# Optimization experiments

Hardware: AMD Instinct MI355X
Metric: run time of the kernel (lower is better)

Reference implementation:

```python
import jax, jax.numpy as jnp
import numpy as np

L = 10   # lattice side (hardcoded self.length)
K = 3    # kernel_size -> half_k = 1 wrap padding
FN = 4   # filter_num
B = 262144


def setup_inputs() -> dict:
    key = jax.random.key(0)
    k1, k2, k3, k4, k5 = jax.random.split(key, 5)
    v = jax.random.normal(k1, (B, L * L), dtype=jnp.float32)
    # torch default init scale ~ 1/sqrt(fan_in)
    conv_w = jax.random.normal(k2, (FN, 1, K, K), dtype=jnp.float32) / 3.0
    conv_b = jax.random.normal(k3, (FN,), dtype=jnp.float32) * 0.1
    deconv_w = jax.random.normal(k4, (FN, 1, 2, 2), dtype=jnp.float32) / 4.0
    deconv_b = jax.random.normal(k5, (1,), dtype=jnp.float32) * 0.1
    data = jnp.zeros((1,), dtype=jnp.int32)  # unused positional arg of log_psi
    return {"v": v, "conv_w": conv_w, "conv_b": conv_b,
            "deconv_w": deconv_w, "deconv_b": deconv_b, "data": data}


def _log_psi(v, conv_w, conv_b, deconv_w, deconv_b):
    b = v.shape[0]
    x = v.reshape(b, 1, L, L)
    # handmade_padding == periodic (wrap) pad of width half_k=1 on both spatial axes
    x = jnp.pad(x, ((0, 0), (0, 0), (1, 1), (1, 1)), mode="wrap")  # [B,1,12,12]
    # Conv2d(1, FN, 3), VALID -> [B,FN,10,10]
    y = jax.lax.conv_general_dilated(
        x, conv_w, window_strides=(1, 1), padding="VALID",
        dimension_numbers=("NCHW", "OIHW", "NCHW"))
    y = y + conv_b[None, :, None, None]
    # MaxPool2d(2,2): non-overlapping 2x2 -> [B,FN,5,5]
    y = y.reshape(b, FN, L // 2, 2, L // 2, 2).max(axis=(3, 5))
    # ConvTranspose2d(FN,1,kernel=2,stride=2): each input pixel -> disjoint 2x2 block
    # torch weight layout [in=FN, out=1, 2, 2]
    z = jnp.einsum("bcij,cokl->boikjl", y, deconv_w).reshape(b, 1, L, L)
    z = z + deconv_b[None, :, None, None]
    sign_z = jnp.sign(z)
    abs_z = z * sign_z
    sign_prod = sign_z.reshape(b, -1).prod(axis=1)        # scalar per sample
    log_sum = jnp.log(abs_z).reshape(b, -1).sum(axis=1)   # scalar per sample
    return sign_prod, log_sum


def reference(v, conv_w, conv_b, deconv_w, deconv_b, data):
    return _log_psi(v, conv_w, conv_b, deconv_w, deconv_b)
```

## Files before the change

### kernel.cpp

```cpp
#include <hip/hip_runtime.h>
#include <math.h>


#define SREAD(x) __int_as_float(__builtin_amdgcn_readfirstlane(__float_as_int(x)))

__global__ __launch_bounds__(128) void CNN2D_37495064494620_kernel(
    const float* __restrict__ v,
    const float* __restrict__ cw,
    const float* __restrict__ cb,
    const float* __restrict__ dw,
    const float* __restrict__ db,
    float* __restrict__ out,
    int B)
{
    const int tid = threadIdx.x;
    const int b = blockIdx.x * 128 + tid;

    __shared__ __align__(16) float sm[128 * 100];

    const float* gbase = v + (size_t)blockIdx.x * 12800;
    const int widx = tid >> 6;
    #pragma unroll
    for (int k = 0; k < 25; ++k) {
        __builtin_amdgcn_global_load_lds(
            (const __attribute__((address_space(1))) void*)(gbase + k * 512 + tid * 4),
            (__attribute__((address_space(3))) void*)&sm[k * 512 + widx * 256],
            16, 0, 0);
    }

    float W[4][9];
    #pragma unroll
    for (int f = 0; f < 4; ++f)
        #pragma unroll
        for (int t = 0; t < 9; ++t)
            W[f][t] = SREAD(cw[f * 9 + t]);
    float Cb[4];
    #pragma unroll
    for (int f = 0; f < 4; ++f) Cb[f] = SREAD(cb[f]);
    float Dw[4][4];
    #pragma unroll
    for (int f = 0; f < 4; ++f)
        #pragma unroll
        for (int t = 0; t < 4; ++t)
            Dw[f][t] = SREAD(dw[f * 4 + t]);
    const float Db = SREAD(db[0]);

    __syncthreads();

    const int myoff = tid * 100;
    unsigned sbits = 0u;
    float l2 = 0.0f;

    #pragma clang loop unroll(disable)
    for (int i = 0; i < 5; ++i) {
        const int rows[4] = { (i == 0) ? 9 : 2 * i - 1,
                              2 * i,
                              2 * i + 1,
                              (i == 4) ? 0 : 2 * i + 2 };
        float R[4][10];
        #pragma unroll
        for (int rr = 0; rr < 4; ++rr) {
            const int base = myoff + rows[rr] * 10;
            #pragma unroll
            for (int t = 0; t < 5; ++t) {
                float2 q = *(const float2*)&sm[base + 2 * t];
                R[rr][2 * t]     = q.x;
                R[rr][2 * t + 1] = q.y;
            }
        }
        #pragma unroll
        for (int j = 0; j < 5; ++j) {
            float p0, p1, p2, p3;
            #pragma unroll
            for (int dr = 0; dr < 2; ++dr) {
                #pragma unroll
                for (int dc = 0; dc < 2; ++dc) {
                    float a0 = Cb[0], a1 = Cb[1], a2 = Cb[2], a3 = Cb[3];
                    #pragma unroll
                    for (int kr = 0; kr < 3; ++kr) {
                        #pragma unroll
                        for (int kc = 0; kc < 3; ++kc) {
                            const int cc = (2 * j + dc + kc + 9) % 10;
                            const float xv = R[dr + kr][cc];
                            const int t = kr * 3 + kc;
                            a0 = fmaf(xv, W[0][t], a0);
                            a1 = fmaf(xv, W[1][t], a1);
                            a2 = fmaf(xv, W[2][t], a2);
                            a3 = fmaf(xv, W[3][t], a3);
                        }
                    }
                    if (dr == 0 && dc == 0) {
                        p0 = a0; p1 = a1; p2 = a2; p3 = a3;
                    } else {
                        p0 = fmaxf(p0, a0); p1 = fmaxf(p1, a1);
                        p2 = fmaxf(p2, a2); p3 = fmaxf(p3, a3);
                    }
                }
            }
            float z[4];
            #pragma unroll
            for (int kl = 0; kl < 4; ++kl) {
                float zz = Db;
                zz = fmaf(p0, Dw[0][kl], zz);
                zz = fmaf(p1, Dw[1][kl], zz);
                zz = fmaf(p2, Dw[2][kl], zz);
                zz = fmaf(p3, Dw[3][kl], zz);
                z[kl] = zz;
                sbits ^= __float_as_uint(zz);
            }
            l2 += __log2f(fabsf(z[0] * z[1])) + __log2f(fabsf(z[2] * z[3]));
        }
    }

    out[b]     = (sbits & 0x80000000u) ? -1.0f : 1.0f;
    out[B + b] = l2 * 0.69314718055994531f;
}

extern "C" void kernel_launch(void* const* d_in, const int* in_sizes, int n_in,
                              void* d_out, int out_size, void* d_ws, size_t ws_size,
                              hipStream_t stream) {
    const float* v  = (const float*)d_in[0];
    const float* cw = (const float*)d_in[1];
    const float* cb = (const float*)d_in[2];
    const float* dw = (const float*)d_in[3];
    const float* db = (const float*)d_in[4];
    float* out = (float*)d_out;

    const int B = in_sizes[0] / 100;
    const int grid = (B + 127) / 128;
    CNN2D_37495064494620_kernel<<<grid, 128, 0, stream>>>(v, cw, cb, dw, db, out, B);
}
```

Before: 182.2 us.

## Split each sample across two lanes and pool rows via lane shuffle

Each sample is now handled by a pair of lanes: each lane computes the convolution for one of the two rows in every pooling window, and the lanes combine their maxima with a cross-lane shuffle. Blocks shrink to 64 threads covering 32 samples, which cuts LDS per block and is meant to fit more waves per CU and hide latency better. The outer row loop is also fully unrolled. The cost is duplicated deconvolution and log work in both lanes, plus a shuffle per pooled value.

```diff
diff --git a/kernel.cpp b/kernel.cpp
--- a/kernel.cpp
+++ b/kernel.cpp
@@ -4,7 +4,18 @@
 
 #define SREAD(x) __int_as_float(__builtin_amdgcn_readfirstlane(__float_as_int(x)))
 
-__global__ __launch_bounds__(128) void CNN2D_37495064494620_kernel(
+__device__ __forceinline__ void gload16(const float* g, float* l) {
+    __builtin_amdgcn_global_load_lds(
+        (const __attribute__((address_space(1))) void*)g,
+        (__attribute__((address_space(3))) void*)l, 16, 0, 0);
+}
+__device__ __forceinline__ void gload4(const float* g, float* l) {
+    __builtin_amdgcn_global_load_lds(
+        (const __attribute__((address_space(1))) void*)g,
+        (__attribute__((address_space(3))) void*)l, 4, 0, 0);
+}
+
+__global__ __launch_bounds__(64) void CNN2D_37495064494620_kernel(
     const float* __restrict__ v,
     const float* __restrict__ cw,
     const float* __restrict__ cb,
@@ -13,20 +24,19 @@
     float* __restrict__ out,
     int B)
 {
-    const int tid = threadIdx.x;
-    const int b = blockIdx.x * 128 + tid;
+    const int l  = threadIdx.x;
+    const int q  = l & 1;
+    const int sl = l >> 1;
 
-    __shared__ __align__(16) float sm[128 * 100];
+    __shared__ __align__(16) float sm[3200];
 
-    const float* gbase = v + (size_t)blockIdx.x * 12800;
-    const int widx = tid >> 6;
+    const float* gbase = v + (size_t)blockIdx.x * 3200;
     #pragma unroll
-    for (int k = 0; k < 25; ++k) {
-        __builtin_amdgcn_global_load_lds(
-            (const __attribute__((address_space(1))) void*)(gbase + k * 512 + tid * 4),
-            (__attribute__((address_space(3))) void*)&sm[k * 512 + widx * 256],
-            16, 0, 0);
-    }
+    for (int k = 0; k < 12; ++k)
+        gload16(gbase + k * 256 + l * 4, &sm[k * 256]);
+    #pragma unroll
+    for (int k = 0; k < 2; ++k)
+        gload4(gbase + 3072 + k * 64 + l, &sm[3072 + k * 64]);
 
     float W[4][9];
     #pragma unroll
@@ -47,64 +57,71 @@
 
     __syncthreads();
 
-    const int myoff = tid * 100;
+    const float* my = sm + sl * 100;
+
     unsigned sbits = 0u;
     float l2 = 0.0f;
 
-    #pragma clang loop unroll(disable)
+    #pragma unroll
     for (int i = 0; i < 5; ++i) {
-        const int rows[4] = { (i == 0) ? 9 : 2 * i - 1,
-                              2 * i,
-                              2 * i + 1,
-                              (i == 4) ? 0 : 2 * i + 2 };
-        float R[4][10];
+        const int r1 = 2 * i + q;
+        const int r0 = (i == 0) ? (q ? 0 : 9) : (2 * i - 1 + q);
+        const int r2 = (i == 4) ? (q ? 0 : 9) : (2 * i + 1 + q);
+
+        float R[3][10];
         #pragma unroll
-        for (int rr = 0; rr < 4; ++rr) {
-            const int base = myoff + rows[rr] * 10;
-            #pragma unroll
-            for (int t = 0; t < 5; ++t) {
-                float2 q = *(const float2*)&sm[base + 2 * t];
-                R[rr][2 * t]     = q.x;
-                R[rr][2 * t + 1] = q.y;
-            }
+        for (int t = 0; t < 5; ++t) {
+            float2 x0 = *(const float2*)(my + r0 * 10 + 2 * t);
+            float2 x1 = *(const float2*)(my + r1 * 10 + 2 * t);
+            float2 x2 = *(const float2*)(my + r2 * 10 + 2 * t);
+            R[0][2 * t] = x0.x; R[0][2 * t + 1] = x0.y;
+            R[1][2 * t] = x1.x; R[1][2 * t + 1] = x1.y;
+            R[2][2 * t] = x2.x; R[2][2 * t + 1] = x2.y;
         }
+
+        float M[5][4];
         #pragma unroll
         for (int j = 0; j < 5; ++j) {
-            float p0, p1, p2, p3;
+            float a0[4], a1[4];
             #pragma unroll
-            for (int dr = 0; dr < 2; ++dr) {
+            for (int f = 0; f < 4; ++f) { a0[f] = Cb[f]; a1[f] = Cb[f]; }
+            #pragma unroll
+            for (int kr = 0; kr < 3; ++kr) {
                 #pragma unroll
-                for (int dc = 0; dc < 2; ++dc) {
-                    float a0 = Cb[0], a1 = Cb[1], a2 = Cb[2], a3 = Cb[3];
+                for (int kc = 0; kc < 3; ++kc) {
+                    const int cc0 = (2 * j + kc + 9) % 10;
+                    const int cc1 = (2 * j + 1 + kc + 9) % 10;
+                    const float x0 = R[kr][cc0];
+                    const float x1 = R[kr][cc1];
+                    const int t = kr * 3 + kc;
                     #pragma unroll
-                    for (int kr = 0; kr < 3; ++kr) {
-                        #pragma unroll
-                        for (int kc = 0; kc < 3; ++kc) {
-                            const int cc = (2 * j + dc + kc + 9) % 10;
-                            const float xv = R[dr + kr][cc];
-                            const int t = kr * 3 + kc;
-                            a0 = fmaf(xv, W[0][t], a0);
-                            a1 = fmaf(xv, W[1][t], a1);
-                            a2 = fmaf(xv, W[2][t], a2);
-                            a3 = fmaf(xv, W[3][t], a3);
-                        }
-                    }
-                    if (dr == 0 && dc == 0) {
-                        p0 = a0; p1 = a1; p2 = a2; p3 = a3;
-                    } else {
-                        p0 = fmaxf(p0, a0); p1 = fmaxf(p1, a1);
-                        p2 = fmaxf(p2, a2); p3 = fmaxf(p3, a3);
+                    for (int f = 0; f < 4; ++f) {
+                        a0[f] = fmaf(x0, W[f][t], a0[f]);
+                        a1[f] = fmaf(x1, W[f][t], a1[f]);
                     }
                 }
             }
+            #pragma unroll
+            for (int f = 0; f < 4; ++f)
+                M[j][f] = fmaxf(a0[f], a1[f]);
+        }
+
+        float P[5][4];
+        #pragma unroll
+        for (int j = 0; j < 5; ++j)
+            #pragma unroll
+            for (int f = 0; f < 4; ++f)
+                P[j][f] = fmaxf(M[j][f], __shfl_xor(M[j][f], 1));
+
+        #pragma unroll
+        for (int j = 0; j < 5; ++j) {
             float z[4];
             #pragma unroll
             for (int kl = 0; kl < 4; ++kl) {
                 float zz = Db;
-                zz = fmaf(p0, Dw[0][kl], zz);
-                zz = fmaf(p1, Dw[1][kl], zz);
-                zz = fmaf(p2, Dw[2][kl], zz);
-                zz = fmaf(p3, Dw[3][kl], zz);
+                #pragma unroll
+                for (int f = 0; f < 4; ++f)
+                    zz = fmaf(P[j][f], Dw[f][kl], zz);
                 z[kl] = zz;
                 sbits ^= __float_as_uint(zz);
             }
@@ -112,8 +129,10 @@
         }
     }
 
-    out[b]     = (sbits & 0x80000000u) ? -1.0f : 1.0f;
-    out[B + b] = l2 * 0.69314718055994531f;
+    const int s = blockIdx.x * 32 + sl;
+    const float val = q ? (l2 * 0.69314718055994531f)
+                        : ((sbits & 0x80000000u) ? -1.0f : 1.0f);
+    out[q * B + s] = val;
 }
 
 extern "C" void kernel_launch(void* const* d_in, const int* in_sizes, int n_in,
@@ -127,6 +146,6 @@
     float* out = (float*)d_out;
 
     const int B = in_sizes[0] / 100;
-    const int grid = (B + 127) / 128;
-    CNN2D_37495064494620_kernel<<<grid, 128, 0, stream>>>(v, cw, cb, dw, db, out, B);
+    const int grid = B / 32;
+    CNN2D_37495064494620_kernel<<<grid, 64, 0, stream>>>(v, cw, cb, dw, db, out, B);
 }
```

New measurement: 169.3 us. -7.1%, faster.

## Split each sample across lane pairs and software-pipeline sample tiles through LDS

Applied to the files above, without the earlier changes.

Each sample is now processed by two adjacent lanes: one handles the even conv rows and the other the odd rows, and the 2x2 max-pool is completed with a DPP lane swap. Each block loops over four tiles of 64 samples, prefetching the next tile into registers while the current tile is computed from LDS. This replaces the async global-to-LDS load. The change halves per-thread work and registers per sample, and overlaps global loads with compute. In exchange it adds extra syncthreads, uses more registers for the prefetch buffer, and the grid B/256 assumes B is divisible by 256.

```diff
diff --git a/kernel.cpp b/kernel.cpp
--- a/kernel.cpp
+++ b/kernel.cpp
@@ -3,6 +3,69 @@
 
 
 #define SREAD(x) __int_as_float(__builtin_amdgcn_readfirstlane(__float_as_int(x)))
+
+__device__ __forceinline__ float dpp_swap1_f(float x) {
+    return __int_as_float(__builtin_amdgcn_mov_dpp(__float_as_int(x), 0xB1, 0xF, 0xF, true));
+}
+__device__ __forceinline__ unsigned dpp_swap1_u(unsigned x) {
+    return (unsigned)__builtin_amdgcn_mov_dpp((int)x, 0xB1, 0xF, 0xF, true);
+}
+
+__device__ __forceinline__ void ldrow(float (&R)[10], const float* p) {
+    #pragma unroll
+    for (int t = 0; t < 5; ++t) {
+        float2 x = *(const float2*)(p + 2 * t);
+        R[2 * t] = x.x; R[2 * t + 1] = x.y;
+    }
+}
+
+__device__ __forceinline__ void step(
+    const float (&X)[10], const float (&Y)[10], const float (&Z)[10],
+    const float (&W)[4][9], const float (&Cb)[4],
+    const float (&Dq0)[4], const float (&Dq1)[4], const float Db,
+    unsigned& sbits, float& l2)
+{
+    #pragma unroll
+    for (int j = 0; j < 5; ++j) {
+        float a[4], b[4];
+        #pragma unroll
+        for (int f = 0; f < 4; ++f) { a[f] = Cb[f]; b[f] = Cb[f]; }
+        #pragma unroll
+        for (int kc = 0; kc < 3; ++kc) {
+            const int c0 = (2 * j + kc + 9) % 10;
+            const int c1 = (2 * j + 1 + kc + 9) % 10;
+            #pragma unroll
+            for (int f = 0; f < 4; ++f) {
+                a[f] = fmaf(X[c0], W[f][kc], a[f]);
+                b[f] = fmaf(X[c1], W[f][kc], b[f]);
+            }
+            #pragma unroll
+            for (int f = 0; f < 4; ++f) {
+                a[f] = fmaf(Y[c0], W[f][3 + kc], a[f]);
+                b[f] = fmaf(Y[c1], W[f][3 + kc], b[f]);
+            }
+            #pragma unroll
+            for (int f = 0; f < 4; ++f) {
+                a[f] = fmaf(Z[c0], W[f][6 + kc], a[f]);
+                b[f] = fmaf(Z[c1], W[f][6 + kc], b[f]);
+            }
+        }
+        float P[4];
+        #pragma unroll
+        for (int f = 0; f < 4; ++f) {
+            const float m = fmaxf(a[f], b[f]);
+            P[f] = fmaxf(m, dpp_swap1_f(m));
+        }
+        float z0 = Db, z1 = Db;
+        #pragma unroll
+        for (int f = 0; f < 4; ++f) {
+            z0 = fmaf(P[f], Dq0[f], z0);
+            z1 = fmaf(P[f], Dq1[f], z1);
+        }
+        sbits ^= __float_as_uint(z0) ^ __float_as_uint(z1);
+        l2 += __log2f(fabsf(z0 * z1));
+    }
+}
 
 __global__ __launch_bounds__(128) void CNN2D_37495064494620_kernel(
     const float* __restrict__ v,
@@ -14,19 +77,10 @@
     int B)
 {
     const int tid = threadIdx.x;
-    const int b = blockIdx.x * 128 + tid;
+    const int q   = tid & 1;
+    const int sl  = tid >> 1;
 
-    __shared__ __align__(16) float sm[128 * 100];
-
-    const float* gbase = v + (size_t)blockIdx.x * 12800;
-    const int widx = tid >> 6;
-    #pragma unroll
-    for (int k = 0; k < 25; ++k) {
-        __builtin_amdgcn_global_load_lds(
-            (const __attribute__((address_space(1))) void*)(gbase + k * 512 + tid * 4),
-            (__attribute__((address_space(3))) void*)&sm[k * 512 + widx * 256],
-            16, 0, 0);
-    }
+    __shared__ __align__(16) float sm[6400];
 
     float W[4][9];
     #pragma unroll
@@ -44,76 +98,66 @@
         for (int t = 0; t < 4; ++t)
             Dw[f][t] = SREAD(dw[f * 4 + t]);
     const float Db = SREAD(db[0]);
+    float Dq0[4], Dq1[4];
+    #pragma unroll
+    for (int f = 0; f < 4; ++f) {
+        Dq0[f] = q ? Dw[f][2] : Dw[f][0];
+        Dq1[f] = q ? Dw[f][3] : Dw[f][1];
+    }
 
-    __syncthreads();
-
-    const int myoff = tid * 100;
-    unsigned sbits = 0u;
-    float l2 = 0.0f;
+    float2 PF[25];
+    {
+        const float2* g = (const float2*)(v + (size_t)blockIdx.x * 4 * 6400);
+        #pragma unroll
+        for (int k = 0; k < 25; ++k) PF[k] = g[k * 128 + tid];
+    }
 
     #pragma clang loop unroll(disable)
-    for (int i = 0; i < 5; ++i) {
-        const int rows[4] = { (i == 0) ? 9 : 2 * i - 1,
-                              2 * i,
-                              2 * i + 1,
-                              (i == 4) ? 0 : 2 * i + 2 };
-        float R[4][10];
+    for (int n = 0; n < 4; ++n) {
+        const int t = blockIdx.x * 4 + n;
+
+        __syncthreads();
+
         #pragma unroll
-        for (int rr = 0; rr < 4; ++rr) {
-            const int base = myoff + rows[rr] * 10;
+        for (int k = 0; k < 25; ++k)
+            *(float2*)&sm[k * 256 + tid * 2] = PF[k];
+
+        if (n < 3) {
+            const float2* g = (const float2*)(v + (size_t)(t + 1) * 6400);
             #pragma unroll
-            for (int t = 0; t < 5; ++t) {
-                float2 q = *(const float2*)&sm[base + 2 * t];
-                R[rr][2 * t]     = q.x;
-                R[rr][2 * t + 1] = q.y;
-            }
+            for (int k = 0; k < 25; ++k) PF[k] = g[k * 128 + tid];
         }
-        #pragma unroll
-        for (int j = 0; j < 5; ++j) {
-            float p0, p1, p2, p3;
-            #pragma unroll
-            for (int dr = 0; dr < 2; ++dr) {
-                #pragma unroll
-                for (int dc = 0; dc < 2; ++dc) {
-                    float a0 = Cb[0], a1 = Cb[1], a2 = Cb[2], a3 = Cb[3];
-                    #pragma unroll
-                    for (int kr = 0; kr < 3; ++kr) {
-                        #pragma unroll
-                        for (int kc = 0; kc < 3; ++kc) {
-                            const int cc = (2 * j + dc + kc + 9) % 10;
-                            const float xv = R[dr + kr][cc];
-                            const int t = kr * 3 + kc;
-                            a0 = fmaf(xv, W[0][t], a0);
-                            a1 = fmaf(xv, W[1][t], a1);
-                            a2 = fmaf(xv, W[2][t], a2);
-                            a3 = fmaf(xv, W[3][t], a3);
-                        }
-                    }
-                    if (dr == 0 && dc == 0) {
-                        p0 = a0; p1 = a1; p2 = a2; p3 = a3;
-                    } else {
-                        p0 = fmaxf(p0, a0); p1 = fmaxf(p1, a1);
-                        p2 = fmaxf(p2, a2); p3 = fmaxf(p3, a3);
-                    }
-                }
-            }
-            float z[4];
-            #pragma unroll
-            for (int kl = 0; kl < 4; ++kl) {
-                float zz = Db;
-                zz = fmaf(p0, Dw[0][kl], zz);
-                zz = fmaf(p1, Dw[1][kl], zz);
-                zz = fmaf(p2, Dw[2][kl], zz);
-                zz = fmaf(p3, Dw[3][kl], zz);
-                z[kl] = zz;
-                sbits ^= __float_as_uint(zz);
-            }
-            l2 += __log2f(fabsf(z[0] * z[1])) + __log2f(fabsf(z[2] * z[3]));
-        }
+
+        __syncthreads();
+
+        const float* my = sm + sl * 100;
+        unsigned sbits = 0u;
+        float l2 = 0.0f;
+
+        float A[10], Br[10], C[10], D[10], E[10], Fr[10], G[10], H[10], I[10], J[10];
+        ldrow(A,  my + 10 * (q ? 0 : 9));
+        ldrow(Br, my + 10 * q);
+        ldrow(C,  my + 10 * (q + 1));
+        step(A, Br, C, W, Cb, Dq0, Dq1, Db, sbits, l2);
+        ldrow(D,  my + 10 * (2 + q));
+        ldrow(E,  my + 10 * (3 + q));
+        step(C, D, E, W, Cb, Dq0, Dq1, Db, sbits, l2);
+        ldrow(Fr, my + 10 * (4 + q));
+        ldrow(G,  my + 10 * (5 + q));
+        step(E, Fr, G, W, Cb, Dq0, Dq1, Db, sbits, l2);
+        ldrow(H,  my + 10 * (6 + q));
+        ldrow(I,  my + 10 * (7 + q));
+        step(G, H, I, W, Cb, Dq0, Dq1, Db, sbits, l2);
+        ldrow(J,  my + 10 * (8 + q));
+        step(I, J, A, W, Cb, Dq0, Dq1, Db, sbits, l2);
+
+        const float l2t = l2 + dpp_swap1_f(l2);
+        const unsigned st = sbits ^ dpp_swap1_u(sbits);
+        const int s = t * 64 + sl;
+        const float val = q ? (l2t * 0.69314718055994531f)
+                            : ((st & 0x80000000u) ? -1.0f : 1.0f);
+        out[q * B + s] = val;
     }
-
-    out[b]     = (sbits & 0x80000000u) ? -1.0f : 1.0f;
-    out[B + b] = l2 * 0.69314718055994531f;
 }
 
 extern "C" void kernel_launch(void* const* d_in, const int* in_sizes, int n_in,
@@ -127,6 +171,6 @@
     float* out = (float*)d_out;
 
     const int B = in_sizes[0] / 100;
-    const int grid = (B + 127) / 128;
+    const int grid = B / 256;
     CNN2D_37495064494620_kernel<<<grid, 128, 0, stream>>>(v, cw, cb, dw, db, out, B);
 }
```

Result: no change. 183.5 us (+0.7%).
